# Kernel optimization log

Measured on AMD Instinct MI355X. Metric: run time of the kernel, lower is better.

The kernel has to match this reference:

```python
import jax, jax.numpy as jnp
import numpy as np
from jax import lax

# GlobalSeed with a standard Mamba2 (SSD) core.
# C=64 feature channels, G=8 token dim, d_inner=16, d_state=16, nheads=2, headdim=8, d_conv=3.
C_FEAT, G, D_INNER, D_STATE, NHEADS, HEADDIM, D_CONV = 64, 8, 16, 16, 2, 8, 3
CONV_DIM = D_INNER + 2 * D_STATE  # 48
D_IN_PROJ = 2 * D_INNER + 2 * D_STATE + NHEADS  # 66


def setup_inputs() -> dict:
    key = jax.random.key(0)
    ks = jax.random.split(key, 16)
    B, H, W = 16, 128, 128
    s = 0.02
    return {
        "x": jax.random.normal(ks[0], (B, C_FEAT, H, W), jnp.float32),
        "tok_w": s * jax.random.normal(ks[1], (G, C_FEAT), jnp.float32),
        "tok_b": jnp.zeros((G,), jnp.float32),
        "detok_w": s * jax.random.normal(ks[2], (C_FEAT, G), jnp.float32),
        "detok_b": jnp.zeros((C_FEAT,), jnp.float32),
        "in_proj_w": s * jax.random.normal(ks[3], (D_IN_PROJ, G), jnp.float32),
        "in_proj_b": jnp.zeros((D_IN_PROJ,), jnp.float32),
        "conv_w": s * jax.random.normal(ks[4], (CONV_DIM, D_CONV), jnp.float32),
        "conv_b": jnp.zeros((CONV_DIM,), jnp.float32),
        "A_log": jnp.log(jnp.arange(1, NHEADS + 1, dtype=jnp.float32)),
        "D": jnp.ones((NHEADS,), jnp.float32),
        "dt_bias": 0.1 * jax.random.normal(ks[5], (NHEADS,), jnp.float32),
        "norm_w": jnp.ones((D_INNER,), jnp.float32),
        "out_w": s * jax.random.normal(ks[6], (G, D_INNER), jnp.float32),
        "out_b": jnp.zeros((G,), jnp.float32),
    }


def _mamba2(gt, in_proj_w, in_proj_b, conv_w, conv_b, A_log, D, dt_bias, norm_w, out_w, out_b):
    # gt: (B, L, G) tokens
    B, L, _ = gt.shape
    zxbcdt = gt @ in_proj_w.T + in_proj_b  # (B, L, 66)
    z = zxbcdt[..., :D_INNER]
    xBC = zxbcdt[..., D_INNER:D_INNER + CONV_DIM]
    dt = zxbcdt[..., D_INNER + CONV_DIM:]  # (B, L, nheads)
    # depthwise causal conv1d over L
    xBC = lax.conv_general_dilated(
        xBC.transpose(0, 2, 1), conv_w[:, None, :], (1,), [(D_CONV - 1, 0)],
        feature_group_count=CONV_DIM).transpose(0, 2, 1) + conv_b
    xBC = jax.nn.silu(xBC)
    xr = xBC[..., :D_INNER].reshape(B, L, NHEADS, HEADDIM)
    Bm = xBC[..., D_INNER:D_INNER + D_STATE]   # (B, L, N)
    Cm = xBC[..., D_INNER + D_STATE:]          # (B, L, N)
    dt = jax.nn.softplus(dt + dt_bias)          # (B, L, H)
    dec = jnp.exp(dt * (-jnp.exp(A_log)))       # (B, L, H)

    def step(h, inp):
        xt, Bt, Ct, dtt, dct = inp  # (B,H,P) (B,N) (B,N) (B,H) (B,H)
        h = dct[:, :, None, None] * h + (dtt[:, :, None] * xt)[..., None] * Bt[:, None, None, :]
        y = jnp.einsum('bhpn,bn->bhp', h, Ct)
        return h, y

    h0 = jnp.zeros((B, NHEADS, HEADDIM, D_STATE), gt.dtype)
    xs = (xr.transpose(1, 0, 2, 3), Bm.transpose(1, 0, 2), Cm.transpose(1, 0, 2),
          dt.transpose(1, 0, 2), dec.transpose(1, 0, 2))
    _, ys = lax.scan(step, h0, xs)  # (L, B, H, P)
    y = ys.transpose(1, 0, 2, 3) + D[None, None, :, None] * xr
    y = y.reshape(B, L, D_INNER)
    y = y * jax.nn.silu(z)  # gated
    y = y * lax.rsqrt(jnp.mean(y * y, axis=-1, keepdims=True) + 1e-5) * norm_w  # RMSNormGated
    return y @ out_w.T + out_b  # (B, L, G)


def reference(x, tok_w, tok_b, detok_w, detok_b, in_proj_w, in_proj_b, conv_w, conv_b,
              A_log, D, dt_bias, norm_w, out_w, out_b):
    B, C, H, W = x.shape
    L = H * W
    g = jnp.einsum('bchw,gc->bghw', x, tok_w) + tok_b[None, :, None, None]
    gt = g.reshape(B, G, L).transpose(0, 2, 1)  # (B, L, G)
    gt = _mamba2(gt, in_proj_w, in_proj_b, conv_w, conv_b, A_log, D, dt_bias, norm_w, out_w, out_b) + gt
    g2 = gt.transpose(0, 2, 1).reshape(B, G, H, W)
    return x + jnp.einsum('bghw,cg->bchw', g2, detok_w) + detok_b[None, :, None, None]
```

## Files before the change

kernel.cpp:

```cpp
#include <hip/hip_runtime.h>
#include <math.h>

#define NB 16
#define CF 64
#define LL 16384
#define GG 8
#define NH 2
#define CHN 64
#define NCH 256
#define NGRP 16

static constexpr size_t OFF_GT = 0;
static constexpr size_t OFF_U2 = OFF_GT + (size_t)NB*LL*GG;
static constexpr size_t OFF_AC = OFF_U2 + (size_t)NB*NCH*256;
static constexpr size_t OFF_PH = OFF_AC + (size_t)NB*NCH*NH;
static constexpr size_t OFF_CP = OFF_PH + (size_t)NB*NCH*256;
static constexpr size_t OFF_UG = OFF_CP + (size_t)NB*NCH*NH;
static constexpr size_t OFF_AG = OFF_UG + (size_t)NB*NGRP*256;
static constexpr size_t OFF_GH = OFF_AG + (size_t)NB*NGRP*NH;
static constexpr size_t OFF_G2 = OFF_GH + (size_t)NB*NGRP*256;
static constexpr size_t WS_FLOATS = OFF_G2 + (size_t)NB*LL*GG;

typedef float f32x4 __attribute__((ext_vector_type(4)));
typedef short bf16x8 __attribute__((ext_vector_type(8)));

__device__ __forceinline__ float siluf(float v){ return v / (1.f + __expf(-v)); }
__device__ __forceinline__ float softplusf(float v){ return v > 20.f ? v : log1pf(__expf(v)); }

__device__ __forceinline__ unsigned short f2bf(float f){
    unsigned int u = __float_as_uint(f);
    u += 0x7fffu + ((u >> 16) & 1u);
    return (unsigned short)(u >> 16);
}
__device__ __forceinline__ float bf2f(unsigned short s){
    return __uint_as_float(((unsigned int)s) << 16);
}
__device__ __forceinline__ unsigned int pack2bf(float lo, float hi){
    return (unsigned int)f2bf(lo) | ((unsigned int)f2bf(hi) << 16);
}

__device__ __forceinline__ void load8(float* d, const float* p){
    float4 a = ((const float4*)p)[0];
    float4 b = ((const float4*)p)[1];
    d[0]=a.x; d[1]=a.y; d[2]=a.z; d[3]=a.w;
    d[4]=b.x; d[5]=b.y; d[6]=b.z; d[7]=b.w;
}

__global__ __launch_bounds__(64) void k1a_tok(
    const float* __restrict__ x, const float* __restrict__ tok_w,
    const float* __restrict__ tok_b, float* __restrict__ gtw)
{
    __shared__ float s_tok[GG*CF];
    int tid = threadIdx.x;
    int b  = blockIdx.x >> 6;
    int ck = blockIdx.x & 63;
    int l0 = (ck << 8) + (tid << 2);
    for (int i = tid; i < GG*CF; i += 64) s_tok[i] = tok_w[i];
    __syncthreads();
    float acc[4][GG];
    #pragma unroll
    for (int r = 0; r < 4; ++r)
        #pragma unroll
        for (int g = 0; g < GG; ++g) acc[r][g] = tok_b[g];
    const float* xb = x + (size_t)b*CF*LL + l0;
    #pragma unroll 8
    for (int c = 0; c < CF; ++c) {
        float4 xv = *(const float4*)(xb + (size_t)c*LL);
        float xa[4] = {xv.x, xv.y, xv.z, xv.w};
        #pragma unroll
        for (int g = 0; g < GG; ++g) {
            float w = s_tok[g*CF + c];
            #pragma unroll
            for (int r = 0; r < 4; ++r) acc[r][g] = fmaf(xa[r], w, acc[r][g]);
        }
    }
    float* gp = gtw + ((size_t)b*LL + l0)*GG;
    #pragma unroll
    for (int r = 0; r < 4; ++r) {
        ((float4*)gp)[r*2+0] = make_float4(acc[r][0],acc[r][1],acc[r][2],acc[r][3]);
        ((float4*)gp)[r*2+1] = make_float4(acc[r][4],acc[r][5],acc[r][6],acc[r][7]);
    }
}

__global__ __launch_bounds__(256) void k2a_state(
    const float* __restrict__ gtw,
    const float* __restrict__ ipw, const float* __restrict__ ipb,
    const float* __restrict__ cw, const float* __restrict__ cb,
    const float* __restrict__ A_log, const float* __restrict__ dt_bias,
    float* __restrict__ U2w, float* __restrict__ Acw)
{
    __shared__ __align__(16) unsigned short XTbf[16*72];
    __shared__ __align__(16) unsigned short BTbf[16*72];
    __shared__ __align__(16) unsigned short WXbf[16*72];
    __shared__ float s_dt[64][2], s_nda[64][2];
    __shared__ float s_ipw[256], s_ipb2[32], s_cw2[96], s_cb2[32], s_wdt[16];

    int tid = threadIdx.x;
    int b = blockIdx.x >> 8, c = blockIdx.x & 255;
    s_ipw[tid] = ipw[128 + tid];
    if (tid < 32) { s_ipb2[tid] = ipb[16 + tid]; s_cb2[tid] = cb[tid]; }
    else if (tid >= 64 && tid < 160) s_cw2[tid - 64] = cw[tid - 64];
    else if (tid >= 224 && tid < 240) s_wdt[tid - 224] = ipw[512 + (tid - 224)];
    __syncthreads();

    float a0e = __expf(A_log[0]), a1e = __expf(A_log[1]);
    float dtb0 = dt_bias[0], dtb1 = dt_bias[1];
    float bdt0 = ipb[64], bdt1 = ipb[65];

    {
        int r = tid >> 2, sub = tid & 3;
        int l = c*CHN + r;
        size_t gb = ((size_t)b*LL + l)*GG;
        float g0[8], g1[8], g2v[8];
        #pragma unroll
        for (int g = 0; g < 8; ++g) { g1[g] = 0.f; g2v[g] = 0.f; }
        load8(g0, gtw + gb);
        if (l >= 1) load8(g1, gtw + gb - GG);
        if (l >= 2) load8(g2v, gtw + gb - 2*GG);
        #pragma unroll
        for (int k = 0; k < 8; ++k) {
            int ch = sub*8 + k;
            float bia = s_ipb2[ch];
            float tA = bia, tB = bia, tC = bia;
            #pragma unroll
            for (int g = 0; g < 8; ++g) {
                float wv = s_ipw[ch*8+g];
                tA = fmaf(g0[g],  wv, tA);
                tB = fmaf(g1[g],  wv, tB);
                tC = fmaf(g2v[g], wv, tC);
            }
            if (l < 1) tB = 0.f;
            if (l < 2) tC = 0.f;
            float a = s_cb2[ch];
            a = fmaf(tC, s_cw2[ch*3+0], a);
            a = fmaf(tB, s_cw2[ch*3+1], a);
            a = fmaf(tA, s_cw2[ch*3+2], a);
            float v = siluf(a);
            if (ch < 16) XTbf[ch*72 + r] = f2bf(v);
            else         BTbf[(ch-16)*72 + r] = f2bf(v);
        }
        if (sub == 0) {
            float d0 = bdt0, d1 = bdt1;
            #pragma unroll
            for (int g = 0; g < 8; ++g) {
                d0 = fmaf(g0[g], s_wdt[g],   d0);
                d1 = fmaf(g0[g], s_wdt[8+g], d1);
            }
            float dt0 = softplusf(d0 + dtb0), dt1 = softplusf(d1 + dtb1);
            s_dt[r][0] = dt0; s_dt[r][1] = dt1;
            s_nda[r][0] = -dt0*a0e; s_nda[r][1] = -dt1*a1e;
        }
    }
    __syncthreads();

    if (tid < 64) {
        int rr = tid;
        float v0 = s_nda[rr][0], v1 = s_nda[rr][1];
        #pragma unroll
        for (int off = 1; off < 64; off <<= 1) {
            float t0 = __shfl_up(v0, off);
            float t1 = __shfl_up(v1, off);
            if (rr >= off) { v0 += t0; v1 += t1; }
        }
        float f0 = __shfl(v0, 63), f1 = __shfl(v1, 63);
        float w0 = __expf(f0 - v0) * s_dt[rr][0];
        float w1 = __expf(f1 - v1) * s_dt[rr][1];
        if (rr == 63)
            *(float2*)(Acw + ((size_t)b*NCH + c)*2) = make_float2(__expf(f0), __expf(f1));
        #pragma unroll
        for (int pp = 0; pp < 16; ++pp) {
            float wh = (pp < 8) ? w0 : w1;
            WXbf[pp*72 + rr] = f2bf(wh * bf2f(XTbf[pp*72 + rr]));
        }
        int ar = tid & 15, kb = tid >> 4;
        f32x4 acc = {0.f, 0.f, 0.f, 0.f};
        #pragma unroll
        for (int kk = 0; kk < 2; ++kk) {
            bf16x8 aw = *(const bf16x8*)&WXbf[ar*72 + kk*32 + kb*8];
            bf16x8 bb = *(const bf16x8*)&BTbf[ar*72 + kk*32 + kb*8];
            acc = __builtin_amdgcn_mfma_f32_16x16x32_bf16(aw, bb, acc, 0, 0, 0);
        }
        #pragma unroll
        for (int rg = 0; rg < 4; ++rg)
            U2w[(((size_t)b*NCH + c) << 8) + (kb*4+rg)*16 + ar] = acc[rg];
    }
}

__global__ void k4c1(const float* __restrict__ U2w, const float* __restrict__ Acw,
                     float* __restrict__ phw, float* __restrict__ cpw,
                     float* __restrict__ Ugw, float* __restrict__ Agw)
{
    int b = blockIdx.x >> 4, grp = blockIdx.x & 15;
    int e = threadIdx.x, he = e >> 7;
    size_t base = (size_t)b*NCH + grp*16;
    float u[16], A[16];
    #pragma unroll
    for (int j = 0; j < 16; ++j) u[j] = U2w[((base + j) << 8) + e];
    #pragma unroll
    for (int j = 0; j < 16; ++j) A[j] = Acw[(base + j)*2 + he];
    float h = 0.f, cp = 1.f;
    #pragma unroll
    for (int j = 0; j < 16; ++j) {
        phw[((base + j) << 8) + e] = h;
        if ((e & 127) == 0) cpw[(base + j)*2 + he] = cp;
        h = fmaf(A[j], h, u[j]);
        cp *= A[j];
    }
    Ugw[(((size_t)b*NGRP + grp) << 8) + e] = h;
    if ((e & 127) == 0) Agw[((size_t)b*NGRP + grp)*2 + he] = cp;
}

__global__ void k4c2(const float* __restrict__ Ugw, const float* __restrict__ Agw,
                     float* __restrict__ ghw)
{
    int b = blockIdx.x, e = threadIdx.x, he = e >> 7;
    float u[NGRP], ag[NGRP];
    #pragma unroll
    for (int g = 0; g < NGRP; ++g) {
        u[g]  = Ugw[(((size_t)b*NGRP + g) << 8) + e];
        ag[g] = Agw[((size_t)b*NGRP + g)*2 + he];
    }
    float h = 0.f;
    #pragma unroll
    for (int g = 0; g < NGRP; ++g) {
        ghw[(((size_t)b*NGRP + g) << 8) + e] = h;
        h = fmaf(ag[g], h, u[g]);
    }
}

__global__ __launch_bounds__(256) void k2b_fused(
    const float* __restrict__ gtw,
    const float* __restrict__ ipw, const float* __restrict__ ipb,
    const float* __restrict__ cw, const float* __restrict__ cb,
    const float* __restrict__ A_log, const float* __restrict__ dt_bias,
    const float* __restrict__ Dv, const float* __restrict__ norm_w,
    const float* __restrict__ out_w, const float* __restrict__ out_b,
    const float* __restrict__ phw, const float* __restrict__ cpw,
    const float* __restrict__ ghw,
    float* __restrict__ g2w)
{
    __shared__ __align__(16) unsigned short Cbf[64*40];
    __shared__ __align__(16) unsigned short Bbf[64*40];
    __shared__ __align__(16) unsigned short XTbf[16*72];
    __shared__ __align__(16) unsigned short Mbf[64*72];
    __shared__ __align__(16) unsigned short Cp0[64*16];
    __shared__ __align__(16) unsigned short Cp1[64*16];
    __shared__ float s_hin[256];
    __shared__ float s_dt[64][2], s_nda[64][2], s_la[64][2];
    __shared__ float s_ipw[384], s_ipb2[48], s_cw2[144], s_cb2[48], s_wdt[16];
    __shared__ float s_zw[128], s_ow[128];

    int tid = threadIdx.x;
    int b = blockIdx.x >> 8, c = blockIdx.x & 255;

    {
        int grp = c >> 4;
        float gh  = ghw[(((size_t)b*NGRP + grp) << 8) + tid];
        float cpv = cpw[((size_t)b*NCH + c)*2 + (tid >> 7)];
        float phv = phw[(((size_t)b*NCH + c) << 8) + tid];
        s_hin[tid] = fmaf(cpv, gh, phv);
    }
    for (int i = tid; i < 384; i += 256) s_ipw[i] = ipw[128 + i];
    if (tid < 128) s_zw[tid] = ipw[tid];
    else s_ow[tid-128] = out_w[tid-128];
    if (tid < 48) { s_ipb2[tid] = ipb[16 + tid]; s_cb2[tid] = cb[tid]; }
    else if (tid >= 64 && tid < 208) s_cw2[tid - 64] = cw[tid - 64];
    else if (tid >= 224 && tid < 240) s_wdt[tid - 224] = ipw[512 + (tid - 224)];
    __syncthreads();

    float a0e = __expf(A_log[0]), a1e = __expf(A_log[1]);
    float dtb0 = dt_bias[0], dtb1 = dt_bias[1];
    float bdt0 = ipb[64], bdt1 = ipb[65];
    float D0 = Dv[0], D1 = Dv[1];

    {
        int r = tid >> 2, sub = tid & 3;
        int l = c*CHN + r;
        size_t gb = ((size_t)b*LL + l)*GG;
        float g0[8], g1[8], g2v[8];
        #pragma unroll
        for (int g = 0; g < 8; ++g) { g1[g] = 0.f; g2v[g] = 0.f; }
        load8(g0, gtw + gb);
        if (l >= 1) load8(g1, gtw + gb - GG);
        if (l >= 2) load8(g2v, gtw + gb - 2*GG);
        #pragma unroll
        for (int k = 0; k < 12; ++k) {
            int ch = sub*12 + k;
            float bia = s_ipb2[ch];
            float tA = bia, tB = bia, tC = bia;
            #pragma unroll
            for (int g = 0; g < 8; ++g) {
                float wv = s_ipw[ch*8+g];
                tA = fmaf(g0[g],  wv, tA);
                tB = fmaf(g1[g],  wv, tB);
                tC = fmaf(g2v[g], wv, tC);
            }
            if (l < 1) tB = 0.f;
            if (l < 2) tC = 0.f;
            float a = s_cb2[ch];
            a = fmaf(tC, s_cw2[ch*3+0], a);
            a = fmaf(tB, s_cw2[ch*3+1], a);
            a = fmaf(tA, s_cw2[ch*3+2], a);
            float v = siluf(a);
            if (ch < 16)      XTbf[ch*72 + r] = f2bf(v);
            else if (ch < 32) Bbf[r*40 + (ch-16)] = f2bf(v);
            else              Cbf[r*40 + (ch-32)] = f2bf(v);
        }
        unsigned int* cz = (unsigned int*)&Cbf[r*40 + 16];
        unsigned int* bz = (unsigned int*)&Bbf[r*40 + 16];
        cz[sub*2+0] = 0u; cz[sub*2+1] = 0u;
        bz[sub*2+0] = 0u; bz[sub*2+1] = 0u;
        if (sub == 0) {
            float d0 = bdt0, d1 = bdt1;
            #pragma unroll
            for (int g = 0; g < 8; ++g) {
                d0 = fmaf(g0[g], s_wdt[g],   d0);
                d1 = fmaf(g0[g], s_wdt[8+g], d1);
            }
            float dt0 = softplusf(d0 + dtb0), dt1 = softplusf(d1 + dtb1);
            s_dt[r][0] = dt0; s_dt[r][1] = dt1;
            s_nda[r][0] = -dt0*a0e; s_nda[r][1] = -dt1*a1e;
        }
    }
    __syncthreads();

    int lane = tid & 63, wv = tid >> 6;
    int ar = lane & 15, kb = lane >> 4;
    int trow = wv*16 + kb*4;

    f32x4 gT[4];
    {
        bf16x8 aC = *(const bf16x8*)&Cbf[(wv*16 + ar)*40 + kb*8];
        #pragma unroll
        for (int ss = 0; ss < 4; ++ss) {
            f32x4 g = {0.f, 0.f, 0.f, 0.f};
            if (ss <= wv) {
                bf16x8 bB = *(const bf16x8*)&Bbf[(ss*16 + ar)*40 + kb*8];
                g = __builtin_amdgcn_mfma_f32_16x16x32_bf16(aC, bB, g, 0, 0, 0);
            }
            gT[ss] = g;
        }
    }
    if (tid < 64) {
        int rr = tid;
        float v0 = s_nda[rr][0], v1 = s_nda[rr][1];
        #pragma unroll
        for (int off = 1; off < 64; off <<= 1) {
            float t0 = __shfl_up(v0, off);
            float t1 = __shfl_up(v1, off);
            if (rr >= off) { v0 += t0; v1 += t1; }
        }
        s_la[rr][0] = v0; s_la[rr][1] = v1;
    }
    __syncthreads();

    {
        int h = tid >> 7;
        int rr = (tid & 127) >> 1;
        int nh = (tid & 1) * 8;
        float sc = __expf(s_la[rr][h]);
        unsigned short* Cp = h ? Cp1 : Cp0;
        unsigned int* dst = (unsigned int*)&Cp[rr*16 + nh];
        #pragma unroll
        for (int j = 0; j < 4; ++j)
            dst[j] = pack2bf(sc * bf2f(Cbf[rr*40 + nh + j*2]),
                             sc * bf2f(Cbf[rr*40 + nh + j*2 + 1]));
    }
    float lr0 = s_la[wv*16][0], lr1 = s_la[wv*16][1];
    float ef0[4], ef1[4];
    #pragma unroll
    for (int rg = 0; rg < 4; ++rg) {
        ef0[rg] = __expf(s_la[trow+rg][0] - lr0);
        ef1[rg] = __expf(s_la[trow+rg][1] - lr1);
    }
    {
        for (int ss = 0; ss < 4; ++ss) {
            int s = ss*16 + ar;
            if (ss > wv) {
                if (!(ar & 1)) {
                    #pragma unroll
                    for (int rg = 0; rg < 4; ++rg)
                        *(unsigned int*)&Mbf[(trow+rg)*72 + ss*16 + ar] = 0u;
                }
                continue;
            }
            float ec0 = __expf(lr0 - s_la[s][0]) * s_dt[s][0];
            #pragma unroll
            for (int rg = 0; rg < 4; ++rg) {
                float m = (s <= trow+rg) ? ef0[rg]*ec0*gT[ss][rg] : 0.f;
                float mp = __shfl_xor(m, 1);
                if (!(ar & 1))
                    *(unsigned int*)&Mbf[(trow+rg)*72 + ss*16 + ar] = pack2bf(m, mp);
            }
        }
    }
    __syncthreads();

    f32x4 acc0 = {0.f, 0.f, 0.f, 0.f};
    {
        int p = ar;
        #pragma unroll
        for (int kk = 0; kk < 2; ++kk) {
            bf16x8 am = *(const bf16x8*)&Mbf[(wv*16 + ar)*72 + kk*32 + kb*8];
            bf16x8 bx = {0,0,0,0,0,0,0,0};
            if (p < 8) bx = *(const bf16x8*)&XTbf[p*72 + kk*32 + kb*8];
            acc0 = __builtin_amdgcn_mfma_f32_16x16x32_bf16(am, bx, acc0, 0, 0, 0);
        }
        bf16x8 aCp = {0,0,0,0,0,0,0,0};
        if (kb < 2) aCp = *(const bf16x8*)&Cp0[(wv*16 + ar)*16 + kb*8];
        bf16x8 bh = {0,0,0,0,0,0,0,0};
        if (kb < 2) {
            #pragma unroll
            for (int j = 0; j < 8; ++j)
                bh[j] = (short)f2bf(s_hin[0*128 + (ar&7)*16 + kb*8 + j]);
        }
        acc0 = __builtin_amdgcn_mfma_f32_16x16x32_bf16(aCp, bh, acc0, 0, 0, 0);
    }
    __syncthreads();

    {
        for (int ss = 0; ss < 4; ++ss) {
            int s = ss*16 + ar;
            if (ss > wv) {
                if (!(ar & 1)) {
                    #pragma unroll
                    for (int rg = 0; rg < 4; ++rg)
                        *(unsigned int*)&Mbf[(trow+rg)*72 + ss*16 + ar] = 0u;
                }
                continue;
            }
            float ec1 = __expf(lr1 - s_la[s][1]) * s_dt[s][1];
            #pragma unroll
            for (int rg = 0; rg < 4; ++rg) {
                float m = (s <= trow+rg) ? ef1[rg]*ec1*gT[ss][rg] : 0.f;
                float mp = __shfl_xor(m, 1);
                if (!(ar & 1))
                    *(unsigned int*)&Mbf[(trow+rg)*72 + ss*16 + ar] = pack2bf(m, mp);
            }
        }
    }
    __syncthreads();

    float* yb = (float*)Cbf;
    {
        int p = ar;
        f32x4 acc1 = {0.f, 0.f, 0.f, 0.f};
        #pragma unroll
        for (int kk = 0; kk < 2; ++kk) {
            bf16x8 am = *(const bf16x8*)&Mbf[(wv*16 + ar)*72 + kk*32 + kb*8];
            bf16x8 bx = {0,0,0,0,0,0,0,0};
            if (p < 8) bx = *(const bf16x8*)&XTbf[(8 + p)*72 + kk*32 + kb*8];
            acc1 = __builtin_amdgcn_mfma_f32_16x16x32_bf16(am, bx, acc1, 0, 0, 0);
        }
        bf16x8 aCp = {0,0,0,0,0,0,0,0};
        if (kb < 2) aCp = *(const bf16x8*)&Cp1[(wv*16 + ar)*16 + kb*8];
        bf16x8 bh = {0,0,0,0,0,0,0,0};
        if (kb < 2) {
            #pragma unroll
            for (int j = 0; j < 8; ++j)
                bh[j] = (short)f2bf(s_hin[1*128 + (ar&7)*16 + kb*8 + j]);
        }
        acc1 = __builtin_amdgcn_mfma_f32_16x16x32_bf16(aCp, bh, acc1, 0, 0, 0);
        if (p < 8) {
            #pragma unroll
            for (int rg = 0; rg < 4; ++rg) {
                int t = trow + rg;
                yb[t*20 + p]     = fmaf(D0, bf2f(XTbf[p*72 + t]),     acc0[rg]);
                yb[t*20 + 8 + p] = fmaf(D1, bf2f(XTbf[(8+p)*72 + t]), acc1[rg]);
            }
        }
    }
    __syncthreads();

    {
        int r = tid >> 2, q = tid & 3;
        float gv[8]; load8(gv, gtw + ((size_t)b*LL + c*CHN + r)*GG);
        float vv[4]; float ssq = 0.f;
        #pragma unroll
        for (int j = 0; j < 4; ++j) {
            int hp = q*4 + j;
            float zz = ipb[hp];
            #pragma unroll
            for (int g = 0; g < 8; ++g) zz = fmaf(gv[g], s_zw[hp*8+g], zz);
            float y = yb[r*20 + hp];
            float w = y * siluf(zz);
            vv[j] = w; ssq = fmaf(w, w, ssq);
        }
        ssq += __shfl_xor(ssq, 1);
        ssq += __shfl_xor(ssq, 2);
        float rn = rsqrtf(ssq*(1.f/16.f) + 1e-5f);
        float o[8];
        #pragma unroll
        for (int g = 0; g < 8; ++g) o[g] = 0.f;
        #pragma unroll
        for (int j = 0; j < 4; ++j) {
            float wj = vv[j] * rn * norm_w[q*4+j];
            #pragma unroll
            for (int g = 0; g < 8; ++g) o[g] = fmaf(wj, s_ow[g*16 + q*4 + j], o[g]);
        }
        #pragma unroll
        for (int g = 0; g < 8; ++g) {
            o[g] += __shfl_xor(o[g], 1);
            o[g] += __shfl_xor(o[g], 2);
        }
        if (q == 0) {
            #pragma unroll
            for (int g = 0; g < 8; ++g) o[g] += out_b[g] + gv[g];
            float* gp = g2w + ((size_t)b*LL + c*CHN + r)*GG;
            ((float4*)gp)[0] = make_float4(o[0],o[1],o[2],o[3]);
            ((float4*)gp)[1] = make_float4(o[4],o[5],o[6],o[7]);
        }
    }
}

__global__ __launch_bounds__(64) void k5b_detok(
    const float* __restrict__ x, const float* __restrict__ g2w,
    const float* __restrict__ dkw, const float* __restrict__ dkb,
    float* __restrict__ outp)
{
    __shared__ float s_dw[CF*GG];
    __shared__ float s_db[CF];
    int tid = threadIdx.x;
    int b  = blockIdx.x >> 6;
    int ck = blockIdx.x & 63;
    int l0 = (ck << 8) + (tid << 2);
    for (int i = tid; i < CF*GG; i += 64) s_dw[i] = dkw[i];
    s_db[tid] = dkb[tid];
    __syncthreads();
    float g2v[4][8];
    const float* gp = g2w + ((size_t)b*LL + l0)*GG;
    #pragma unroll
    for (int r = 0; r < 4; ++r) load8(g2v[r], gp + r*GG);
    const float* xb = x + (size_t)b*CF*LL + l0;
    float* ob = outp + (size_t)b*CF*LL + l0;
    #pragma unroll 4
    for (int c = 0; c < CF; ++c) {
        float4 xv = *(const float4*)(xb + (size_t)c*LL);
        float bias = s_db[c];
        float oa[4] = {xv.x+bias, xv.y+bias, xv.z+bias, xv.w+bias};
        #pragma unroll
        for (int g = 0; g < GG; ++g) {
            float w = s_dw[c*GG+g];
            #pragma unroll
            for (int r = 0; r < 4; ++r) oa[r] = fmaf(g2v[r][g], w, oa[r]);
        }
        *(float4*)(ob + (size_t)c*LL) = make_float4(oa[0],oa[1],oa[2],oa[3]);
    }
}

extern "C" void kernel_launch(void* const* d_in, const int* in_sizes, int n_in,
                              void* d_out, int out_size, void* d_ws, size_t ws_size,
                              hipStream_t stream) {
    const float* x       = (const float*)d_in[0];
    const float* tok_w   = (const float*)d_in[1];
    const float* tok_b   = (const float*)d_in[2];
    const float* detok_w = (const float*)d_in[3];
    const float* detok_b = (const float*)d_in[4];
    const float* ipw     = (const float*)d_in[5];
    const float* ipb     = (const float*)d_in[6];
    const float* cw      = (const float*)d_in[7];
    const float* cb      = (const float*)d_in[8];
    const float* A_log   = (const float*)d_in[9];
    const float* Dv      = (const float*)d_in[10];
    const float* dt_bias = (const float*)d_in[11];
    const float* norm_w  = (const float*)d_in[12];
    const float* out_w   = (const float*)d_in[13];
    const float* out_b   = (const float*)d_in[14];
    float* ws = (float*)d_ws;
    float* outp = (float*)d_out;

    if (ws_size < WS_FLOATS * sizeof(float)) return;

    k1a_tok<<<NB*64, 64, 0, stream>>>(x, tok_w, tok_b, ws+OFF_GT);
    k2a_state<<<NB*NCH, 256, 0, stream>>>(ws+OFF_GT, ipw, ipb, cw, cb,
        A_log, dt_bias, ws+OFF_U2, ws+OFF_AC);
    k4c1<<<NB*NGRP, 256, 0, stream>>>(ws+OFF_U2, ws+OFF_AC,
        ws+OFF_PH, ws+OFF_CP, ws+OFF_UG, ws+OFF_AG);
    k4c2<<<NB, 256, 0, stream>>>(ws+OFF_UG, ws+OFF_AG, ws+OFF_GH);
    k2b_fused<<<NB*NCH, 256, 0, stream>>>(ws+OFF_GT, ipw, ipb, cw, cb,
        A_log, dt_bias, Dv, norm_w, out_w, out_b,
        ws+OFF_PH, ws+OFF_CP, ws+OFF_GH, ws+OFF_G2);
    k5b_detok<<<NB*64, 64, 0, stream>>>(x, ws+OFF_G2, detok_w, detok_b, outp);
}
```

Before: 137.1 us.

## Stage in_proj outputs in shared memory for conv and precompute decay factors

Both the state and fused kernels now compute the in_proj pre-activations once per token into shared memory, plus two halo tokens, and then apply the causal conv from those values. Before, each thread recomputed the projection for its previous two tokens. The intra-chunk decay mask now uses precomputed per-row and per-column exponentials anchored at 16-token blocks, replacing per-element expf calls. Other changes: vectorized bf16 transposed packing into the MFMA tiles, a shared-memory union to save LDS, a padded M stride, truncating bf16 packing for the mask, and caching small weights in LDS. The extra barriers and higher LDS use may offset some of the savings, and the truncating packing slightly changes rounding.

```diff
diff --git a/kernel.cpp b/kernel.cpp
--- a/kernel.cpp
+++ b/kernel.cpp
@@ -38,6 +38,9 @@
 __device__ __forceinline__ unsigned int pack2bf(float lo, float hi){
     return (unsigned int)f2bf(lo) | ((unsigned int)f2bf(hi) << 16);
 }
+__device__ __forceinline__ unsigned int packtr(float lo, float hi){
+    return (__float_as_uint(hi) & 0xffff0000u) | (__float_as_uint(lo) >> 16);
+}
 
 __device__ __forceinline__ void load8(float* d, const float* p){
     float4 a = ((const float4*)p)[0];
@@ -89,10 +92,12 @@
     const float* __restrict__ A_log, const float* __restrict__ dt_bias,
     float* __restrict__ U2w, float* __restrict__ Acw)
 {
-    __shared__ __align__(16) unsigned short XTbf[16*72];
+    __shared__ float s_pre[32*68];
+    __shared__ float s_xf[64*17];
+    __shared__ float s_bf[64*17];
+    __shared__ __align__(16) unsigned short WXbf[16*72];
     __shared__ __align__(16) unsigned short BTbf[16*72];
-    __shared__ __align__(16) unsigned short WXbf[16*72];
-    __shared__ float s_dt[64][2], s_nda[64][2];
+    __shared__ float s_dt[64][2], s_nda[64][2], s_w[64][2];
     __shared__ float s_ipw[256], s_ipb2[32], s_cw2[96], s_cb2[32], s_wdt[16];
 
     int tid = threadIdx.x;
@@ -107,37 +112,36 @@
     float dtb0 = dt_bias[0], dtb1 = dt_bias[1];
     float bdt0 = ipb[64], bdt1 = ipb[65];
 
-    {
-        int r = tid >> 2, sub = tid & 3;
-        int l = c*CHN + r;
-        size_t gb = ((size_t)b*LL + l)*GG;
-        float g0[8], g1[8], g2v[8];
-        #pragma unroll
-        for (int g = 0; g < 8; ++g) { g1[g] = 0.f; g2v[g] = 0.f; }
-        load8(g0, gtw + gb);
-        if (l >= 1) load8(g1, gtw + gb - GG);
-        if (l >= 2) load8(g2v, gtw + gb - 2*GG);
+    int r = tid >> 2, sub = tid & 3;
+    int l = c*CHN + r;
+    {
+        float g0[8];
+        load8(g0, gtw + ((size_t)b*LL + l)*GG);
         #pragma unroll
         for (int k = 0; k < 8; ++k) {
             int ch = sub*8 + k;
-            float bia = s_ipb2[ch];
-            float tA = bia, tB = bia, tC = bia;
-            #pragma unroll
-            for (int g = 0; g < 8; ++g) {
-                float wv = s_ipw[ch*8+g];
-                tA = fmaf(g0[g],  wv, tA);
-                tB = fmaf(g1[g],  wv, tB);
-                tC = fmaf(g2v[g], wv, tC);
-            }
-            if (l < 1) tB = 0.f;
-            if (l < 2) tC = 0.f;
-            float a = s_cb2[ch];
-            a = fmaf(tC, s_cw2[ch*3+0], a);
-            a = fmaf(tB, s_cw2[ch*3+1], a);
-            a = fmaf(tA, s_cw2[ch*3+2], a);
-            float v = siluf(a);
-            if (ch < 16) XTbf[ch*72 + r] = f2bf(v);
-            else         BTbf[(ch-16)*72 + r] = f2bf(v);
+            float acc = s_ipb2[ch];
+            #pragma unroll
+            for (int g = 0; g < 8; ++g) acc = fmaf(g0[g], s_ipw[ch*8+g], acc);
+            s_pre[ch*68 + r + 2] = acc;
+        }
+        if (r < 2) {
+            int lh = c*CHN - 1 - r, slot = 1 - r;
+            if (lh >= 0) {
+                float gh[8];
+                load8(gh, gtw + ((size_t)b*LL + lh)*GG);
+                #pragma unroll
+                for (int k = 0; k < 8; ++k) {
+                    int ch = sub*8 + k;
+                    float acc = s_ipb2[ch];
+                    #pragma unroll
+                    for (int g = 0; g < 8; ++g) acc = fmaf(gh[g], s_ipw[ch*8+g], acc);
+                    s_pre[ch*68 + slot] = acc;
+                }
+            } else {
+                #pragma unroll
+                for (int k = 0; k < 8; ++k) s_pre[(sub*8+k)*68 + slot] = 0.f;
+            }
         }
         if (sub == 0) {
             float d0 = bdt0, d1 = bdt1;
@@ -153,6 +157,22 @@
     }
     __syncthreads();
 
+    {
+        #pragma unroll
+        for (int k = 0; k < 8; ++k) {
+            int ch = sub*8 + k;
+            float p0 = s_pre[ch*68 + r];
+            float p1 = s_pre[ch*68 + r + 1];
+            float p2 = s_pre[ch*68 + r + 2];
+            float a = s_cb2[ch];
+            a = fmaf(p0, s_cw2[ch*3+0], a);
+            a = fmaf(p1, s_cw2[ch*3+1], a);
+            a = fmaf(p2, s_cw2[ch*3+2], a);
+            float v = siluf(a);
+            if (ch < 16) s_xf[r*17 + ch] = v;
+            else         s_bf[r*17 + (ch-16)] = v;
+        }
+    }
     if (tid < 64) {
         int rr = tid;
         float v0 = s_nda[rr][0], v1 = s_nda[rr][1];
@@ -163,15 +183,39 @@
             if (rr >= off) { v0 += t0; v1 += t1; }
         }
         float f0 = __shfl(v0, 63), f1 = __shfl(v1, 63);
-        float w0 = __expf(f0 - v0) * s_dt[rr][0];
-        float w1 = __expf(f1 - v1) * s_dt[rr][1];
+        s_w[rr][0] = __expf(f0 - v0) * s_dt[rr][0];
+        s_w[rr][1] = __expf(f1 - v1) * s_dt[rr][1];
         if (rr == 63)
             *(float2*)(Acw + ((size_t)b*NCH + c)*2) = make_float2(__expf(f0), __expf(f1));
-        #pragma unroll
-        for (int pp = 0; pp < 16; ++pp) {
-            float wh = (pp < 8) ? w0 : w1;
-            WXbf[pp*72 + rr] = f2bf(wh * bf2f(XTbf[pp*72 + rr]));
-        }
+    }
+    __syncthreads();
+
+    {
+        int half = tid >> 7;
+        int t2 = tid & 127;
+        int p = t2 & 15, seg = t2 >> 4;
+        unsigned int wd[4];
+        if (half == 0) {
+            #pragma unroll
+            for (int j = 0; j < 4; ++j) {
+                int s0 = seg*8 + 2*j, s1 = s0 + 1;
+                float a0 = s_xf[s0*17 + p] * s_w[s0][p>>3];
+                float a1 = s_xf[s1*17 + p] * s_w[s1][p>>3];
+                wd[j] = pack2bf(a0, a1);
+            }
+            *(uint4*)&WXbf[p*72 + seg*8] = make_uint4(wd[0],wd[1],wd[2],wd[3]);
+        } else {
+            #pragma unroll
+            for (int j = 0; j < 4; ++j) {
+                int s0 = seg*8 + 2*j, s1 = s0 + 1;
+                wd[j] = pack2bf(s_bf[s0*17 + p], s_bf[s1*17 + p]);
+            }
+            *(uint4*)&BTbf[p*72 + seg*8] = make_uint4(wd[0],wd[1],wd[2],wd[3]);
+        }
+    }
+    __syncthreads();
+
+    if (tid < 64) {
         int ar = tid & 15, kb = tid >> 4;
         f32x4 acc = {0.f, 0.f, 0.f, 0.f};
         #pragma unroll
@@ -227,6 +271,16 @@
         h = fmaf(ag[g], h, u[g]);
     }
 }
+
+struct MMp {
+    unsigned short M[64*80];
+    unsigned short Cp0[64*16];
+    unsigned short Cp1[64*16];
+};
+union SharedU {
+    float pre[48*68];
+    MMp m;
+};
 
 __global__ __launch_bounds__(256) void k2b_fused(
     const float* __restrict__ gtw,
@@ -242,13 +296,13 @@
     __shared__ __align__(16) unsigned short Cbf[64*40];
     __shared__ __align__(16) unsigned short Bbf[64*40];
     __shared__ __align__(16) unsigned short XTbf[16*72];
-    __shared__ __align__(16) unsigned short Mbf[64*72];
-    __shared__ __align__(16) unsigned short Cp0[64*16];
-    __shared__ __align__(16) unsigned short Cp1[64*16];
+    __shared__ float s_xf[64*17];
+    __shared__ SharedU su;
     __shared__ float s_hin[256];
     __shared__ float s_dt[64][2], s_nda[64][2], s_la[64][2];
+    __shared__ float s_eti[2][64], s_etd[2][64], s_esc[2][4][4];
     __shared__ float s_ipw[384], s_ipb2[48], s_cw2[144], s_cb2[48], s_wdt[16];
-    __shared__ float s_zw[128], s_ow[128];
+    __shared__ float s_zw[128], s_ow[128], s_zb[16], s_nw[16], s_ob[8];
 
     int tid = threadIdx.x;
     int b = blockIdx.x >> 8, c = blockIdx.x & 255;
@@ -266,6 +320,8 @@
     if (tid < 48) { s_ipb2[tid] = ipb[16 + tid]; s_cb2[tid] = cb[tid]; }
     else if (tid >= 64 && tid < 208) s_cw2[tid - 64] = cw[tid - 64];
     else if (tid >= 224 && tid < 240) s_wdt[tid - 224] = ipw[512 + (tid - 224)];
+    if (tid < 16) { s_zb[tid] = ipb[tid]; s_nw[tid] = norm_w[tid]; }
+    else if (tid < 24) s_ob[tid-16] = out_b[tid-16];
     __syncthreads();
 
     float a0e = __expf(A_log[0]), a1e = __expf(A_log[1]);
@@ -273,54 +329,101 @@
     float bdt0 = ipb[64], bdt1 = ipb[65];
     float D0 = Dv[0], D1 = Dv[1];
 
-    {
-        int r = tid >> 2, sub = tid & 3;
-        int l = c*CHN + r;
-        size_t gb = ((size_t)b*LL + l)*GG;
-        float g0[8], g1[8], g2v[8];
-        #pragma unroll
-        for (int g = 0; g < 8; ++g) { g1[g] = 0.f; g2v[g] = 0.f; }
-        load8(g0, gtw + gb);
-        if (l >= 1) load8(g1, gtw + gb - GG);
-        if (l >= 2) load8(g2v, gtw + gb - 2*GG);
+    int r = tid >> 2, sub = tid & 3;
+    int l = c*CHN + r;
+    float g0[8];
+    {
+        load8(g0, gtw + ((size_t)b*LL + l)*GG);
         #pragma unroll
         for (int k = 0; k < 12; ++k) {
             int ch = sub*12 + k;
-            float bia = s_ipb2[ch];
-            float tA = bia, tB = bia, tC = bia;
+            float acc = s_ipb2[ch];
+            #pragma unroll
+            for (int g = 0; g < 8; ++g) acc = fmaf(g0[g], s_ipw[ch*8+g], acc);
+            su.pre[ch*68 + r + 2] = acc;
+        }
+        if (r < 2) {
+            int lh = c*CHN - 1 - r, slot = 1 - r;
+            if (lh >= 0) {
+                float gh[8];
+                load8(gh, gtw + ((size_t)b*LL + lh)*GG);
+                #pragma unroll
+                for (int k = 0; k < 12; ++k) {
+                    int ch = sub*12 + k;
+                    float acc = s_ipb2[ch];
+                    #pragma unroll
+                    for (int g = 0; g < 8; ++g) acc = fmaf(gh[g], s_ipw[ch*8+g], acc);
+                    su.pre[ch*68 + slot] = acc;
+                }
+            } else {
+                #pragma unroll
+                for (int k = 0; k < 12; ++k) su.pre[(sub*12+k)*68 + slot] = 0.f;
+            }
+        }
+        if (sub == 0) {
+            float d0 = bdt0, d1 = bdt1;
             #pragma unroll
             for (int g = 0; g < 8; ++g) {
-                float wv = s_ipw[ch*8+g];
-                tA = fmaf(g0[g],  wv, tA);
-                tB = fmaf(g1[g],  wv, tB);
-                tC = fmaf(g2v[g], wv, tC);
-            }
-            if (l < 1) tB = 0.f;
-            if (l < 2) tC = 0.f;
+                d0 = fmaf(g0[g], s_wdt[g],   d0);
+                d1 = fmaf(g0[g], s_wdt[8+g], d1);
+            }
+            float dt0 = softplusf(d0 + dtb0), dt1 = softplusf(d1 + dtb1);
+            s_dt[r][0] = dt0; s_dt[r][1] = dt1;
+            s_nda[r][0] = -dt0*a0e; s_nda[r][1] = -dt1*a1e;
+        }
+    }
+    __syncthreads();
+
+    {
+        float vals[12];
+        #pragma unroll
+        for (int k = 0; k < 12; ++k) {
+            int ch = sub*12 + k;
+            float p0 = su.pre[ch*68 + r];
+            float p1 = su.pre[ch*68 + r + 1];
+            float p2 = su.pre[ch*68 + r + 2];
             float a = s_cb2[ch];
-            a = fmaf(tC, s_cw2[ch*3+0], a);
-            a = fmaf(tB, s_cw2[ch*3+1], a);
-            a = fmaf(tA, s_cw2[ch*3+2], a);
-            float v = siluf(a);
-            if (ch < 16)      XTbf[ch*72 + r] = f2bf(v);
-            else if (ch < 32) Bbf[r*40 + (ch-16)] = f2bf(v);
-            else              Cbf[r*40 + (ch-32)] = f2bf(v);
+            a = fmaf(p0, s_cw2[ch*3+0], a);
+            a = fmaf(p1, s_cw2[ch*3+1], a);
+            a = fmaf(p2, s_cw2[ch*3+2], a);
+            vals[k] = siluf(a);
+        }
+        if (sub == 0) {
+            #pragma unroll
+            for (int k = 0; k < 12; ++k) s_xf[r*17 + k] = vals[k];
+        } else if (sub == 1) {
+            #pragma unroll
+            for (int k = 0; k < 4; ++k) s_xf[r*17 + 12 + k] = vals[k];
+            unsigned int* bp = (unsigned int*)&Bbf[r*40];
+            #pragma unroll
+            for (int j = 0; j < 4; ++j) bp[j] = pack2bf(vals[4+2*j], vals[5+2*j]);
+        } else if (sub == 2) {
+            unsigned int* bp = (unsigned int*)&Bbf[r*40 + 8];
+            #pragma unroll
+            for (int j = 0; j < 4; ++j) bp[j] = pack2bf(vals[2*j], vals[1+2*j]);
+            unsigned int* cp = (unsigned int*)&Cbf[r*40];
+            #pragma unroll
+            for (int j = 0; j < 2; ++j) cp[j] = pack2bf(vals[8+2*j], vals[9+2*j]);
+        } else {
+            unsigned int* cp = (unsigned int*)&Cbf[r*40 + 4];
+            #pragma unroll
+            for (int j = 0; j < 6; ++j) cp[j] = pack2bf(vals[2*j], vals[1+2*j]);
         }
         unsigned int* cz = (unsigned int*)&Cbf[r*40 + 16];
         unsigned int* bz = (unsigned int*)&Bbf[r*40 + 16];
         cz[sub*2+0] = 0u; cz[sub*2+1] = 0u;
         bz[sub*2+0] = 0u; bz[sub*2+1] = 0u;
-        if (sub == 0) {
-            float d0 = bdt0, d1 = bdt1;
-            #pragma unroll
-            for (int g = 0; g < 8; ++g) {
-                d0 = fmaf(g0[g], s_wdt[g],   d0);
-                d1 = fmaf(g0[g], s_wdt[8+g], d1);
-            }
-            float dt0 = softplusf(d0 + dtb0), dt1 = softplusf(d1 + dtb1);
-            s_dt[r][0] = dt0; s_dt[r][1] = dt1;
-            s_nda[r][0] = -dt0*a0e; s_nda[r][1] = -dt1*a1e;
-        }
+    }
+    if (tid < 64) {
+        int rr = tid;
+        float v0 = s_nda[rr][0], v1 = s_nda[rr][1];
+        #pragma unroll
+        for (int off = 1; off < 64; off <<= 1) {
+            float t0 = __shfl_up(v0, off);
+            float t1 = __shfl_up(v1, off);
+            if (rr >= off) { v0 += t0; v1 += t1; }
+        }
+        s_la[rr][0] = v0; s_la[rr][1] = v1;
     }
     __syncthreads();
 
@@ -341,56 +444,64 @@
             gT[ss] = g;
         }
     }
-    if (tid < 64) {
-        int rr = tid;
-        float v0 = s_nda[rr][0], v1 = s_nda[rr][1];
-        #pragma unroll
-        for (int off = 1; off < 64; off <<= 1) {
-            float t0 = __shfl_up(v0, off);
-            float t1 = __shfl_up(v1, off);
-            if (rr >= off) { v0 += t0; v1 += t1; }
-        }
-        s_la[rr][0] = v0; s_la[rr][1] = v1;
-    }
-    __syncthreads();
-
+    if (tid < 128) {
+        int p = tid & 15, seg = tid >> 4;
+        unsigned int wd[4];
+        #pragma unroll
+        for (int j = 0; j < 4; ++j) {
+            int s0 = seg*8 + 2*j, s1 = s0 + 1;
+            wd[j] = pack2bf(s_xf[s0*17 + p], s_xf[s1*17 + p]);
+        }
+        *(uint4*)&XTbf[p*72 + seg*8] = make_uint4(wd[0],wd[1],wd[2],wd[3]);
+    } else {
+        int i = tid - 128;
+        int h = i >> 6, s = i & 63;
+        int anc = s & ~15;
+        float d = s_la[anc][h] - s_la[s][h];
+        float et = __expf(d);
+        s_eti[h][s] = __expf(-d);
+        s_etd[h][s] = et * s_dt[s][h];
+        if (i < 32) {
+            int h2 = i >> 4, wt = (i >> 2) & 3, ws = i & 3;
+            s_esc[h2][wt][ws] = (wt >= ws) ? __expf(s_la[wt*16][h2] - s_la[ws*16][h2]) : 0.f;
+        }
+    }
     {
         int h = tid >> 7;
         int rr = (tid & 127) >> 1;
         int nh = (tid & 1) * 8;
         float sc = __expf(s_la[rr][h]);
-        unsigned short* Cp = h ? Cp1 : Cp0;
+        unsigned short* Cp = h ? su.m.Cp1 : su.m.Cp0;
         unsigned int* dst = (unsigned int*)&Cp[rr*16 + nh];
         #pragma unroll
         for (int j = 0; j < 4; ++j)
             dst[j] = pack2bf(sc * bf2f(Cbf[rr*40 + nh + j*2]),
                              sc * bf2f(Cbf[rr*40 + nh + j*2 + 1]));
     }
-    float lr0 = s_la[wv*16][0], lr1 = s_la[wv*16][1];
-    float ef0[4], ef1[4];
-    #pragma unroll
-    for (int rg = 0; rg < 4; ++rg) {
-        ef0[rg] = __expf(s_la[trow+rg][0] - lr0);
-        ef1[rg] = __expf(s_la[trow+rg][1] - lr1);
-    }
-    {
+    __syncthreads();
+
+    {
+        float rowf[4];
+        #pragma unroll
+        for (int rg = 0; rg < 4; ++rg) rowf[rg] = s_eti[0][trow+rg];
+        #pragma unroll
         for (int ss = 0; ss < 4; ++ss) {
             int s = ss*16 + ar;
             if (ss > wv) {
                 if (!(ar & 1)) {
                     #pragma unroll
                     for (int rg = 0; rg < 4; ++rg)
-                        *(unsigned int*)&Mbf[(trow+rg)*72 + ss*16 + ar] = 0u;
+                        *(unsigned int*)&su.m.M[(trow+rg)*80 + ss*16 + ar] = 0u;
                 }
                 continue;
             }
-            float ec0 = __expf(lr0 - s_la[s][0]) * s_dt[s][0];
+            float colf = s_esc[0][wv][ss] * s_etd[0][s];
             #pragma unroll
             for (int rg = 0; rg < 4; ++rg) {
-                float m = (s <= trow+rg) ? ef0[rg]*ec0*gT[ss][rg] : 0.f;
+                float m = (s <= trow+rg) ? rowf[rg]*colf*gT[ss][rg] : 0.f;
                 float mp = __shfl_xor(m, 1);
                 if (!(ar & 1))
-                    *(unsigned int*)&Mbf[(trow+rg)*72 + ss*16 + ar] = pack2bf(m, mp);
+                    *(unsigned int*)&su.m.M[(trow+rg)*80 + ss*16 + ar] = packtr(m, mp);
             }
         }
     }
@@ -401,13 +512,13 @@
         int p = ar;
         #pragma unroll
         for (int kk = 0; kk < 2; ++kk) {
-            bf16x8 am = *(const bf16x8*)&Mbf[(wv*16 + ar)*72 + kk*32 + kb*8];
+            bf16x8 am = *(const bf16x8*)&su.m.M[(wv*16 + ar)*80 + kk*32 + kb*8];
             bf16x8 bx = {0,0,0,0,0,0,0,0};
             if (p < 8) bx = *(const bf16x8*)&XTbf[p*72 + kk*32 + kb*8];
             acc0 = __builtin_amdgcn_mfma_f32_16x16x32_bf16(am, bx, acc0, 0, 0, 0);
         }
         bf16x8 aCp = {0,0,0,0,0,0,0,0};
-        if (kb < 2) aCp = *(const bf16x8*)&Cp0[(wv*16 + ar)*16 + kb*8];
+        if (kb < 2) aCp = *(const bf16x8*)&su.m.Cp0[(wv*16 + ar)*16 + kb*8];
         bf16x8 bh = {0,0,0,0,0,0,0,0};
         if (kb < 2) {
             #pragma unroll
@@ -419,23 +530,27 @@
     __syncthreads();
 
     {
+        float rowf[4];
+        #pragma unroll
+        for (int rg = 0; rg < 4; ++rg) rowf[rg] = s_eti[1][trow+rg];
+        #pragma unroll
         for (int ss = 0; ss < 4; ++ss) {
             int s = ss*16 + ar;
             if (ss > wv) {
                 if (!(ar & 1)) {
                     #pragma unroll
                     for (int rg = 0; rg < 4; ++rg)
-                        *(unsigned int*)&Mbf[(trow+rg)*72 + ss*16 + ar] = 0u;
+                        *(unsigned int*)&su.m.M[(trow+rg)*80 + ss*16 + ar] = 0u;
                 }
                 continue;
             }
-            float ec1 = __expf(lr1 - s_la[s][1]) * s_dt[s][1];
+            float colf = s_esc[1][wv][ss] * s_etd[1][s];
             #pragma unroll
             for (int rg = 0; rg < 4; ++rg) {
-                float m = (s <= trow+rg) ? ef1[rg]*ec1*gT[ss][rg] : 0.f;
+                float m = (s <= trow+rg) ? rowf[rg]*colf*gT[ss][rg] : 0.f;
                 float mp = __shfl_xor(m, 1);
                 if (!(ar & 1))
-                    *(unsigned int*)&Mbf[(trow+rg)*72 + ss*16 + ar] = pack2bf(m, mp);
+                    *(unsigned int*)&su.m.M[(trow+rg)*80 + ss*16 + ar] = packtr(m, mp);
             }
         }
     }
@@ -447,13 +562,13 @@
         f32x4 acc1 = {0.f, 0.f, 0.f, 0.f};
         #pragma unroll
         for (int kk = 0; kk < 2; ++kk) {
-            bf16x8 am = *(const bf16x8*)&Mbf[(wv*16 + ar)*72 + kk*32 + kb*8];
+            bf16x8 am = *(const bf16x8*)&su.m.M[(wv*16 + ar)*80 + kk*32 + kb*8];
             bf16x8 bx = {0,0,0,0,0,0,0,0};
             if (p < 8) bx = *(const bf16x8*)&XTbf[(8 + p)*72 + kk*32 + kb*8];
             acc1 = __builtin_amdgcn_mfma_f32_16x16x32_bf16(am, bx, acc1, 0, 0, 0);
         }
         bf16x8 aCp = {0,0,0,0,0,0,0,0};
-        if (kb < 2) aCp = *(const bf16x8*)&Cp1[(wv*16 + ar)*16 + kb*8];
+        if (kb < 2) aCp = *(const bf16x8*)&su.m.Cp1[(wv*16 + ar)*16 + kb*8];
         bf16x8 bh = {0,0,0,0,0,0,0,0};
         if (kb < 2) {
             #pragma unroll
@@ -465,23 +580,22 @@
             #pragma unroll
             for (int rg = 0; rg < 4; ++rg) {
                 int t = trow + rg;
-                yb[t*20 + p]     = fmaf(D0, bf2f(XTbf[p*72 + t]),     acc0[rg]);
-                yb[t*20 + 8 + p] = fmaf(D1, bf2f(XTbf[(8+p)*72 + t]), acc1[rg]);
-            }
-        }
-    }
-    __syncthreads();
-
-    {
-        int r = tid >> 2, q = tid & 3;
-        float gv[8]; load8(gv, gtw + ((size_t)b*LL + c*CHN + r)*GG);
+                yb[t*20 + p]     = fmaf(D0, s_xf[t*17 + p],     acc0[rg]);
+                yb[t*20 + 8 + p] = fmaf(D1, s_xf[t*17 + 8 + p], acc1[rg]);
+            }
+        }
+    }
+    __syncthreads();
+
+    {
+        int q = sub;
         float vv[4]; float ssq = 0.f;
         #pragma unroll
         for (int j = 0; j < 4; ++j) {
             int hp = q*4 + j;
-            float zz = ipb[hp];
-            #pragma unroll
-            for (int g = 0; g < 8; ++g) zz = fmaf(gv[g], s_zw[hp*8+g], zz);
+            float zz = s_zb[hp];
+            #pragma unroll
+            for (int g = 0; g < 8; ++g) zz = fmaf(g0[g], s_zw[hp*8+g], zz);
             float y = yb[r*20 + hp];
             float w = y * siluf(zz);
             vv[j] = w; ssq = fmaf(w, w, ssq);
@@ -494,7 +608,7 @@
         for (int g = 0; g < 8; ++g) o[g] = 0.f;
         #pragma unroll
         for (int j = 0; j < 4; ++j) {
-            float wj = vv[j] * rn * norm_w[q*4+j];
+            float wj = vv[j] * rn * s_nw[q*4+j];
             #pragma unroll
             for (int g = 0; g < 8; ++g) o[g] = fmaf(wj, s_ow[g*16 + q*4 + j], o[g]);
         }
@@ -505,7 +619,7 @@
         }
         if (q == 0) {
             #pragma unroll
-            for (int g = 0; g < 8; ++g) o[g] += out_b[g] + gv[g];
+            for (int g = 0; g < 8; ++g) o[g] += s_ob[g] + g0[g];
             float* gp = g2w + ((size_t)b*LL + c*CHN + r)*GG;
             ((float4*)gp)[0] = make_float4(o[0],o[1],o[2],o[3]);
             ((float4*)gp)[1] = make_float4(o[4],o[5],o[6],o[7]);
```

Measured after the change: 153.0 us. +11.6%, slower.
